# Kernel optimization log

Measured on AMD Instinct MI355X. Metric: run time of the kernel, lower is better.

## Reference

```python
import jax, jax.numpy as jnp
import numpy as np

E = 384      # EMBEDDING_SIZE
DFF = 1536
H = 6        # NUM_HEADS
D = E // H   # ATTN_DIM_SIZE = 64
T = 256      # SEQ_LEN
L = 6        # NUM_BLOCKS
V = 65       # VOCAB_SIZE
NPOS = 10000.0
B = 128


def _pos_encoding():
    i = jnp.arange(T, dtype=jnp.float32)[:, None]
    k = jnp.arange(E // 2, dtype=jnp.float32)[None, :]
    ang = i / jnp.power(NPOS, 2.0 * k / E)   # [T, E/2]
    pe = jnp.zeros((T, E), dtype=jnp.float32)
    pe = pe.at[:, 0::2].set(jnp.sin(ang))
    pe = pe.at[:, 1::2].set(jnp.cos(ang))
    return pe


def setup_inputs() -> dict:
    key = jax.random.key(0)
    ks = jax.random.split(key, 24)
    s = 0.02
    n = lambda k, shp: (jax.random.normal(k, shp, dtype=jnp.float32) * s)
    inp = {
        'tokens': jax.random.randint(ks[0], (B, T), 0, V),
        'pos_enc': _pos_encoding(),
        'emb': n(ks[1], (V, E)),
        # stacked per-layer params [L, ...]; weights stored as (in, out)
        'Wq': n(ks[2], (L, E, E)), 'bq': jnp.zeros((L, E)),
        'Wk': n(ks[3], (L, E, E)), 'bk': jnp.zeros((L, E)),
        'Wv': n(ks[4], (L, E, E)), 'bv': jnp.zeros((L, E)),
        'Wo': n(ks[5], (L, E, E)), 'bo': jnp.zeros((L, E)),
        'ln1_g': jnp.ones((L, E)), 'ln1_b': jnp.zeros((L, E)),
        'W1': n(ks[6], (L, E, DFF)), 'c1': jnp.zeros((L, DFF)),
        'W2': n(ks[7], (L, DFF, E)), 'c2': jnp.zeros((L, E)),
        'ln2_g': jnp.ones((L, E)), 'ln2_b': jnp.zeros((L, E)),
        'Wl': n(ks[8], (E, V)), 'bl': jnp.zeros((V,)),
    }
    return inp


def _layer_norm(x, g, b, eps=1e-5):
    mu = jnp.mean(x, axis=-1, keepdims=True)
    var = jnp.mean((x - mu) ** 2, axis=-1, keepdims=True)
    return (x - mu) * jax.lax.rsqrt(var + eps) * g + b


def _decoder(tokens, pos_enc, emb, Wq, bq, Wk, bk, Wv, bv, Wo, bo,
             ln1_g, ln1_b, W1, c1, W2, c2, ln2_g, ln2_b, Wl, bl):
    b_, t_ = tokens.shape
    x = emb[tokens] + pos_enc[None, :t_, :]            # [B,T,E]
    causal = jnp.tril(jnp.ones((t_, t_), dtype=bool)) # tril mask
    scale = D ** (-0.5)

    def block(x, p):
        (wq, bq_, wk, bk_, wv, bv_, wo, bo_, g1, be1, w1, c1_, w2, c2_, g2, be2) = p
        h = _layer_norm(x, g1, be1)
        q = (h @ wq + bq_).reshape(b_, t_, H, D)
        k = (h @ wk + bk_).reshape(b_, t_, H, D)
        v = (h @ wv + bv_).reshape(b_, t_, H, D)
        scores = jnp.einsum('bqhd,bkhd->bhqk', q, k) * scale
        scores = jnp.where(causal[None, None], scores, -jnp.inf)
        attn = jax.nn.softmax(scores, axis=-1)
        o = jnp.einsum('bhqk,bkhd->bqhd', attn, v).reshape(b_, t_, E)
        x = x + (o @ wo + bo_)
        h2 = _layer_norm(x, g2, be2)
        x = x + (jax.nn.relu(h2 @ w1 + c1_) @ w2 + c2_)
        return x, None

    params = (Wq, bq, Wk, bk, Wv, bv, Wo, bo, ln1_g, ln1_b, W1, c1, W2, c2, ln2_g, ln2_b)
    x, _ = jax.lax.scan(block, x, params)
    return x @ Wl + bl                                 # [B,T,V]


def reference(tokens, pos_enc, emb, Wq, bq, Wk, bk, Wv, bv, Wo, bo,
              ln1_g, ln1_b, W1, c1, W2, c2, ln2_g, ln2_b, Wl, bl):
    return _decoder(tokens, pos_enc, emb, Wq, bq, Wk, bk, Wv, bv, Wo, bo,
                    ln1_g, ln1_b, W1, c1, W2, c2, ln2_g, ln2_b, Wl, bl)
```

## Files before the change

kernel.cpp:

```cpp
#include <hip/hip_runtime.h>
#include <hip/hip_bf16.h>
#include <stdint.h>

constexpr int E   = 384;
constexpr int DFF = 1536;
constexpr int NH  = 6;
constexpr int HD  = 64;
constexpr int T   = 256;
constexpr int NL  = 6;
constexpr int NV  = 65;
constexpr int BB  = 128;
constexpr int MTOT = BB * T;
constexpr int CB  = 32;

typedef __bf16 bf16;
typedef __attribute__((ext_vector_type(8))) __bf16 bf16x8;
typedef __attribute__((ext_vector_type(4))) __bf16 bf16x4;
typedef __attribute__((ext_vector_type(4))) float floatx4;

__device__ __forceinline__ void gload_lds16(const void* g, void* l) {
    __builtin_amdgcn_global_load_lds(
        (const __attribute__((address_space(1))) void*)g,
        (__attribute__((address_space(3))) void*)l, 16, 0, 0);
}

#define GBM 128
#define GBN 128
#define GBK 64

template <int MODE, int SWAP>
__device__ __forceinline__ void gemm_body(
    char* AsB,
    const bf16* __restrict__ A, int lda,
    const bf16* __restrict__ Bf,
    const float* __restrict__ bias,
    void* __restrict__ Cv, void* __restrict__ Cv2, int ldc,
    int nt, int mt, int Nvalid, int K, int relu)
{
    int tid = threadIdx.x;
    int lane = tid & 63;
    int wid = tid >> 6;
    int wm = wid >> 2, wn = wid & 3;
    int lq = lane >> 4, lr = lane & 15;

    const bf16* Ab = A + (long)mt * GBM * lda;

    int srow = tid >> 3;
    int slot = tid & 7;
    int skc  = (slot ^ (srow & 7)) * 8;
    const bf16* Arow = Ab + (long)srow * lda + skc;
    const long a2 = 64 * (long)lda;
    int wofs = wid * 1024;

    int nk = K / GBK;
    int nks = K / 32;
    const bf16* Bq = Bf + ((long)(nt * 8 + wn * 2) * nks) * 512 + lane * 8;

    floatx4 zero = {0.f, 0.f, 0.f, 0.f};
    floatx4 acc[4][2];
#pragma unroll
    for (int i = 0; i < 4; i++)
#pragma unroll
        for (int j = 0; j < 2; j++) acc[i][j] = zero;

    const char* rp0 = AsB + (wm * 64 + lr) * 128;
    int rx0 = (lq * 16) ^ ((lr & 7) << 4);

    {
        char* base = AsB + wofs;
        gload_lds16(Arow,      base);
        gload_lds16(Arow + a2, base + 8192);
    }
    asm volatile("s_waitcnt vmcnt(0)" ::: "memory");
    __syncthreads();

    for (int ki = 0; ki < nk; ki++) {
        int ib = ki & 1;
        bf16x8 bb[4];
#pragma unroll
        for (int ni = 0; ni < 2; ni++)
#pragma unroll
            for (int kh = 0; kh < 2; kh++)
                bb[ni * 2 + kh] =
                    *(const bf16x8*)(Bq + ((long)ni * nks + 2 * ki + kh) * 512);
        if (ki + 1 < nk) {
            long koff = (long)(ki + 1) * GBK;
            char* base = AsB + (1 - ib) * 16384 + wofs;
            gload_lds16(Arow + koff,      base);
            gload_lds16(Arow + a2 + koff, base + 8192);
        }
        const char* rp = rp0 + ib * 16384;

        bf16x8 af[4];
#pragma unroll
        for (int mi = 0; mi < 4; mi++)
            af[mi] = *(const bf16x8*)(rp + mi * 2048 + rx0);
#pragma unroll
        for (int mi = 0; mi < 4; mi++)
#pragma unroll
            for (int ni = 0; ni < 2; ni++)
                acc[mi][ni] = SWAP
                    ? __builtin_amdgcn_mfma_f32_16x16x32_bf16(bb[ni * 2], af[mi], acc[mi][ni], 0, 0, 0)
                    : __builtin_amdgcn_mfma_f32_16x16x32_bf16(af[mi], bb[ni * 2], acc[mi][ni], 0, 0, 0);
#pragma unroll
        for (int mi = 0; mi < 4; mi++)
            af[mi] = *(const bf16x8*)(rp + mi * 2048 + (rx0 ^ 64));
#pragma unroll
        for (int mi = 0; mi < 4; mi++)
#pragma unroll
            for (int ni = 0; ni < 2; ni++)
                acc[mi][ni] = SWAP
                    ? __builtin_amdgcn_mfma_f32_16x16x32_bf16(bb[ni * 2 + 1], af[mi], acc[mi][ni], 0, 0, 0)
                    : __builtin_amdgcn_mfma_f32_16x16x32_bf16(af[mi], bb[ni * 2 + 1], acc[mi][ni], 0, 0, 0);
        __syncthreads();
    }

    int m0 = mt * GBM, n0 = nt * GBN;
#pragma unroll
    for (int mi = 0; mi < 4; mi++) {
#pragma unroll
        for (int ni = 0; ni < 2; ni++) {
            floatx4 v = acc[mi][ni];
            if (SWAP) {
                int rowL = m0 + wm * 64 + mi * 16 + lr;
                int col0 = n0 + wn * 32 + ni * 16 + lq * 4;
                if (MODE == 5) {
                    bf16x4 pv;
#pragma unroll
                    for (int r = 0; r < 4; r++) pv[r] = (bf16)(v[r] + bias[col0 + r]);
                    *(bf16x4*)((bf16*)Cv + (long)rowL * 768 + col0) = pv;
                } else if (MODE == 1) {
                    bf16* Cp = (bf16*)Cv;
                    bf16x4* ptr = (bf16x4*)(Cp + (long)rowL * ldc + col0);
                    bf16x4 old = *ptr;
                    bf16x4 pv;
#pragma unroll
                    for (int r = 0; r < 4; r++)
                        pv[r] = (bf16)((float)old[r] + v[r] + bias[col0 + r]);
                    *ptr = pv;
                } else if (MODE == 4) {
                    float* Cp = (float*)Cv;
#pragma unroll
                    for (int r = 0; r < 4; r++)
                        if (col0 + r < Nvalid)
                            Cp[(long)rowL * ldc + col0 + r] = v[r] + bias[col0 + r];
                } else {
                    if (col0 < Nvalid) {
                        bf16x4 pv;
#pragma unroll
                        for (int r = 0; r < 4; r++) {
                            float x = v[r] + (bias ? bias[col0 + r] : 0.f);
                            if (relu) x = fmaxf(x, 0.f);
                            pv[r] = (bf16)x;
                        }
                        *(bf16x4*)((bf16*)Cv + (long)rowL * ldc + col0) = pv;
                    }
                }
            } else {
                int row0 = m0 + wm * 64 + mi * 16 + lq * 4;
                int colL = n0 + wn * 32 + ni * 16 + lr;
                float bv = bias[colL];
                bf16x4 pv;
#pragma unroll
                for (int r = 0; r < 4; r++) pv[r] = (bf16)(v[r] + bv);
                int bidx = row0 >> 8, pos = row0 & 255, e = colL - 768;
                *(bf16x4*)((bf16*)Cv2 + (long)bidx * (E * T) + (long)e * T + pos) = pv;
            }
        }
    }
}

template <int MODE>
__global__ __launch_bounds__(512, 6) void k_gemm(
    const bf16* __restrict__ A, int lda,
    const bf16* __restrict__ Bf,
    const float* __restrict__ bias,
    void* __restrict__ Cv, void* __restrict__ Cv2, int ldc,
    int Mtiles, int Ntiles, int Nvalid, int K,
    int relu)
{
    __shared__ __align__(16) char AsB[2 * 16384];

    int nb = gridDim.x;
    int per = nb >> 3;
    int bphys = blockIdx.x;
    int bid = (bphys & 7) * per + (bphys >> 3);

    int nt = bid % Ntiles;
    int mt = bid / Ntiles;

    if (MODE == 5 && nt >= 6)
        gemm_body<5, 0>(AsB, A, lda, Bf, bias, Cv, Cv2, ldc, nt, mt, Nvalid, K, relu);
    else
        gemm_body<MODE, 1>(AsB, A, lda, Bf, bias, Cv, Cv2, ldc, nt, mt, Nvalid, K, relu);
}

__global__ __launch_bounds__(256) void k_attn(
    const bf16* __restrict__ qk, const bf16* __restrict__ vt,
    bf16* __restrict__ o)
{
    int nb = gridDim.x;
    int per = nb >> 3;
    int bphys = blockIdx.x;
    int bid = (bphys & 7) * per + (bphys >> 3);

    int qt = bid & 3; bid >>= 2;
    int h = bid % NH; int b = bid / NH;
    int tid = threadIdx.x;
    int lane = tid & 63;
    int w = tid >> 6;
    int lq = lane >> 4;
    int lr = lane & 15;

    __shared__ __align__(16) bf16 Ks[256 * 72];
    __shared__ __align__(16) bf16 Vs[64 * 264];

    const bf16* qbase = qk + (long)(b * T + qt * 64 + w * 16) * 768 + h * 64;
    const bf16* kbase = qk + (long)(b * T) * 768 + 384 + h * 64;
    const bf16* vbase = vt + ((long)b * E + h * 64) * T;

#pragma unroll
    for (int i = 0; i < 8; i++) {
        int idx = i * 256 + tid;
        int row = idx >> 3, off = (idx & 7) * 8;
        *(bf16x8*)(&Ks[row * 72 + off]) = *(const bf16x8*)(kbase + (long)row * 768 + off);
    }
#pragma unroll
    for (int i = 0; i < 8; i++) {
        int idx = i * 256 + tid;
        int row = idx >> 5, off = (idx & 31) * 8;
        *(bf16x8*)(&Vs[row * 264 + off]) = *(const bf16x8*)(vbase + (long)row * 256 + off);
    }

    bf16x8 aq0 = *(const bf16x8*)(qbase + (long)lr * 768 + lq * 8);
    bf16x8 aq1 = *(const bf16x8*)(qbase + (long)lr * 768 + 32 + lq * 8);

    __syncthreads();

    const int ntmax = qt * 4 + 3;
    floatx4 zero = {0.f, 0.f, 0.f, 0.f};
    floatx4 s[16];
#pragma unroll
    for (int nt = 0; nt < 16; nt++) s[nt] = zero;

#pragma unroll
    for (int nt = 0; nt < 16; nt++) {
        if (nt <= ntmax) {
            const bf16* kp = &Ks[(nt * 16 + lr) * 72 + lq * 8];
            bf16x8 b0 = *(const bf16x8*)(kp);
            bf16x8 b1 = *(const bf16x8*)(kp + 32);
            s[nt] = __builtin_amdgcn_mfma_f32_16x16x32_bf16(aq0, b0, s[nt], 0, 0, 0);
            s[nt] = __builtin_amdgcn_mfma_f32_16x16x32_bf16(aq1, b1, s[nt], 0, 0, 0);
        }
    }

    int trow0 = qt * 64 + w * 16 + lq * 4;
    float m4[4] = {-3e38f, -3e38f, -3e38f, -3e38f};
#pragma unroll
    for (int nt = 0; nt < 16; nt++) {
        if (nt <= ntmax) {
            int tc = nt * 16 + lr;
#pragma unroll
            for (int r = 0; r < 4; r++) {
                float v = s[nt][r] * 0.125f;
                if (tc > trow0 + r) v = -3e38f;
                s[nt][r] = v;
                m4[r] = fmaxf(m4[r], v);
            }
        }
    }
#pragma unroll
    for (int r = 0; r < 4; r++) {
#pragma unroll
        for (int off = 1; off < 16; off <<= 1)
            m4[r] = fmaxf(m4[r], __shfl_xor(m4[r], off, 64));
    }

    float l4[4] = {0.f, 0.f, 0.f, 0.f};
#pragma unroll
    for (int nt = 0; nt < 16; nt++) {
        if (nt <= ntmax) {
#pragma unroll
            for (int r = 0; r < 4; r++) {
                float pv = __expf(s[nt][r] - m4[r]);
                l4[r] += pv;
                s[nt][r] = pv;
            }
        }
    }
#pragma unroll
    for (int r = 0; r < 4; r++) {
#pragma unroll
        for (int off = 1; off < 16; off <<= 1)
            l4[r] += __shfl_xor(l4[r], off, 64);
    }

    __syncthreads();

    bf16* P = Ks + w * (16 * 264);
#pragma unroll
    for (int nt = 0; nt < 16; nt++) {
        if (nt <= ntmax) {
#pragma unroll
            for (int r = 0; r < 4; r++)
                P[(lq * 4 + r) * 264 + nt * 16 + lr] = (bf16)s[nt][r];
        }
    }

    floatx4 oacc[4];
#pragma unroll
    for (int nd = 0; nd < 4; nd++) oacc[nd] = zero;
    const int kkmax = 2 * (qt + 1);
#pragma unroll
    for (int kk = 0; kk < 8; kk++) {
        if (kk < kkmax) {
            bf16x8 ap = *(const bf16x8*)(&P[lr * 264 + kk * 32 + lq * 8]);
#pragma unroll
            for (int nd = 0; nd < 4; nd++) {
                bf16x8 bv = *(const bf16x8*)(&Vs[(nd * 16 + lr) * 264 + kk * 32 + lq * 8]);
                oacc[nd] = __builtin_amdgcn_mfma_f32_16x16x32_bf16(ap, bv, oacc[nd], 0, 0, 0);
            }
        }
    }

#pragma unroll
    for (int r = 0; r < 4; r++) {
        float inv = 1.0f / l4[r];
        long rowg = (long)b * T + trow0 + r;
#pragma unroll
        for (int nd = 0; nd < 4; nd++) {
            o[rowg * E + h * 64 + nd * 16 + lr] = (bf16)(oacc[nd][r] * inv);
        }
    }
}

__global__ void k_ln(const bf16* __restrict__ x, const float* __restrict__ g,
                     const float* __restrict__ b, bf16* __restrict__ h) {
    int row = blockIdx.x * 4 + (threadIdx.x >> 6);
    int lane = threadIdx.x & 63;
    const bf16* xr = x + (long)row * E;
    float v[6];
    float s = 0.f;
#pragma unroll
    for (int i = 0; i < 6; i++) { v[i] = (float)xr[lane + 64 * i]; s += v[i]; }
#pragma unroll
    for (int o = 1; o < 64; o <<= 1) s += __shfl_xor(s, o, 64);
    float mu = s * (1.0f / E);
    float q = 0.f;
#pragma unroll
    for (int i = 0; i < 6; i++) { float d = v[i] - mu; q += d * d; }
#pragma unroll
    for (int o = 1; o < 64; o <<= 1) q += __shfl_xor(q, o, 64);
    float rs = rsqrtf(q * (1.0f / E) + 1e-5f);
    bf16* hr = h + (long)row * E;
#pragma unroll
    for (int i = 0; i < 6; i++) {
        int c = lane + 64 * i;
        hr[c] = (bf16)((v[i] - mu) * rs * g[c] + b[c]);
    }
}

__global__ void k_transpose_frag(const float* __restrict__ W, bf16* __restrict__ Wf,
                                 int K, int N, int NPAD) {
    long idx = (long)blockIdx.x * 256 + threadIdx.x;
    long per = (long)NPAD * K;
    int l = (int)(idx / per);
    long r = idx - (long)l * per;
    int j = (int)(r & 7); r >>= 3;
    int lane = (int)(r & 63); r >>= 6;
    int nks = K / 32;
    int ks = (int)(r % nks);
    int c16 = (int)(r / nks);
    int col = c16 * 16 + (lane & 15);
    int k = ks * 32 + (lane >> 4) * 8 + j;
    Wf[idx] = (col < N) ? (bf16)W[((long)l * K + k) * N + col] : (bf16)0.0f;
}

__global__ void k_transpose_qkv_frag(const float* __restrict__ Wq, const float* __restrict__ Wk,
                                     const float* __restrict__ Wv, bf16* __restrict__ Wf) {
    long idx = (long)blockIdx.x * 256 + threadIdx.x;
    long per = (long)1152 * E;
    int l = (int)(idx / per);
    long r = idx - (long)l * per;
    int j = (int)(r & 7); r >>= 3;
    int lane = (int)(r & 63); r >>= 6;
    int nks = E / 32;
    int ks = (int)(r % nks);
    int c16 = (int)(r / nks);
    int col = c16 * 16 + (lane & 15);
    int k = ks * 32 + (lane >> 4) * 8 + j;
    const float* src;
    int cc;
    if (col < 384)      { src = Wq; cc = col; }
    else if (col < 768) { src = Wk; cc = col - 384; }
    else                { src = Wv; cc = col - 768; }
    Wf[idx] = (bf16)src[((long)l * E + k) * E + cc];
}

__global__ void k_bias_qkv(const float* __restrict__ bq, const float* __restrict__ bk,
                           const float* __restrict__ bv, float* __restrict__ bqkv) {
    int idx = blockIdx.x * 256 + threadIdx.x;
    int l = idx / 1152;
    int j = idx - l * 1152;
    const float* src;
    int jj;
    if (j < 384)      { src = bq; jj = j; }
    else if (j < 768) { src = bk; jj = j - 384; }
    else              { src = bv; jj = j - 768; }
    bqkv[idx] = src[l * E + jj];
}

__global__ void k_embed(const int* __restrict__ tokens, const float* __restrict__ pos,
                        const float* __restrict__ emb, bf16* __restrict__ x) {
    long idx = (long)blockIdx.x * 256 + threadIdx.x;
    int e = (int)(idx % E);
    long bt = idx / E;
    int t = (int)(bt % T);
    int tok = tokens[bt];
    x[idx] = (bf16)(emb[(long)tok * E + e] + pos[(long)t * E + e]);
}

extern "C" void kernel_launch(void* const* d_in, const int* in_sizes, int n_in,
                              void* d_out, int out_size, void* d_ws, size_t ws_size,
                              hipStream_t stream) {
    const int*   tokens = (const int*)d_in[0];
    const float* pos  = (const float*)d_in[1];
    const float* emb  = (const float*)d_in[2];
    const float* Wq   = (const float*)d_in[3];
    const float* bq   = (const float*)d_in[4];
    const float* Wk   = (const float*)d_in[5];
    const float* bk   = (const float*)d_in[6];
    const float* Wv   = (const float*)d_in[7];
    const float* bv   = (const float*)d_in[8];
    const float* Wo   = (const float*)d_in[9];
    const float* bo   = (const float*)d_in[10];
    const float* g1   = (const float*)d_in[11];
    const float* be1  = (const float*)d_in[12];
    const float* W1   = (const float*)d_in[13];
    const float* c1   = (const float*)d_in[14];
    const float* W2   = (const float*)d_in[15];
    const float* c2   = (const float*)d_in[16];
    const float* g2   = (const float*)d_in[17];
    const float* be2  = (const float*)d_in[18];
    const float* Wl   = (const float*)d_in[19];
    const float* bl   = (const float*)d_in[20];

    char* p = (char*)d_ws;
    bf16* x  = (bf16*)p;   p += (long)MTOT * E * 2;
    bf16* h  = (bf16*)p;   p += (long)MTOT * E * 2;
    bf16* qk = (bf16*)p;   p += (long)MTOT * 768 * 2;
    bf16* vt = (bf16*)p;   p += (long)BB * E * T * 2;
    bf16* SP = (bf16*)p;   p += (long)CB * NH * T * T * 2;
    bf16* WqkvF = (bf16*)p; p += (long)NL * 1152 * E * 2;
    bf16* WoF = (bf16*)p;  p += (long)NL * E * E * 2;
    bf16* W1F = (bf16*)p;  p += (long)NL * DFF * E * 2;
    bf16* W2F = (bf16*)p;  p += (long)NL * E * DFF * 2;
    bf16* WlF = (bf16*)p;  p += (long)128 * E * 2;
    float* bqkv = (float*)p; p += (long)NL * 1152 * 4;
    bf16* mid = qk;
    bf16* o   = h;
    (void)SP;

    k_transpose_qkv_frag<<<(NL * 1152 * E) / 256, 256, 0, stream>>>(Wq, Wk, Wv, WqkvF);
    k_transpose_frag<<<(NL * E * E) / 256, 256, 0, stream>>>(Wo, WoF, E, E, E);
    k_transpose_frag<<<(NL * DFF * E) / 256, 256, 0, stream>>>(W1, W1F, E, DFF, DFF);
    k_transpose_frag<<<(NL * E * DFF) / 256, 256, 0, stream>>>(W2, W2F, DFF, E, E);
    k_transpose_frag<<<(128 * E) / 256, 256, 0, stream>>>(Wl, WlF, E, NV, 128);
    k_bias_qkv<<<(NL * 1152) / 256, 256, 0, stream>>>(bq, bk, bv, bqkv);

    k_embed<<<(MTOT * E) / 256, 256, 0, stream>>>(tokens, pos, emb, x);

    for (int l = 0; l < NL; l++) {
        k_ln<<<MTOT / 4, 256, 0, stream>>>(x, g1 + l * E, be1 + l * E, h);
        k_gemm<5><<<256 * 9, 512, 0, stream>>>(h, E, WqkvF + (long)l * 1152 * E,
                                               bqkv + l * 1152, qk, vt, 0,
                                               256, 9, 1152, E, 0);
        k_attn<<<BB * NH * 4, 256, 0, stream>>>(qk, vt, o);
        k_gemm<1><<<256 * 3, 512, 0, stream>>>(o, E, WoF + (long)l * E * E,
                                               bo + l * E, x, nullptr, E,
                                               256, 3, E, E, 0);
        k_ln<<<MTOT / 4, 256, 0, stream>>>(x, g2 + l * E, be2 + l * E, h);
        k_gemm<0><<<256 * 12, 512, 0, stream>>>(h, E, W1F + (long)l * DFF * E,
                                                c1 + l * DFF, mid, nullptr, DFF,
                                                256, 12, DFF, E, 1);
        k_gemm<1><<<256 * 3, 512, 0, stream>>>(mid, DFF, W2F + (long)l * E * DFF,
                                               c2 + l * E, x, nullptr, E,
                                               256, 3, E, DFF, 0);
    }

    k_gemm<4><<<256 * 1, 512, 0, stream>>>(x, E, WlF,
                                           bl, d_out, nullptr, NV,
                                           256, 1, NV, E, 0);
}
```

Before: 1.676 ms.

## Enlarge GEMM M-tile to 256 with 4x2 wave grid and 64x64 warp tiles

Doubles the GEMM block tile from 128x128 to 256x128 and remaps the eight waves to a 4x2 grid, so each wave computes a 64x64 sub-tile with 16 accumulators instead of 8. The B fragments are now loaded in two halves per k-step to limit register use, and the LDS double buffer doubles to 64KB. The aim is more reuse of each B load and fewer blocks, lowering global traffic per FLOP. In exchange, register and LDS pressure rise (occupancy hint lowered to 4) and the grid halves, which may leave fewer waves to hide latency.

```diff
diff --git a/kernel.cpp b/kernel.cpp
--- a/kernel.cpp
+++ b/kernel.cpp
@@ -24,7 +24,7 @@
         (__attribute__((address_space(3))) void*)l, 16, 0, 0);
 }
 
-#define GBM 128
+#define GBM 256
 #define GBN 128
 #define GBK 64
 
@@ -40,7 +40,7 @@
     int tid = threadIdx.x;
     int lane = tid & 63;
     int wid = tid >> 6;
-    int wm = wid >> 2, wn = wid & 3;
+    int wr = wid >> 1, wc = wid & 1;
     int lq = lane >> 4, lr = lane & 15;
 
     const bf16* Ab = A + (long)mt * GBM * lda;
@@ -54,23 +54,20 @@
 
     int nk = K / GBK;
     int nks = K / 32;
-    const bf16* Bq = Bf + ((long)(nt * 8 + wn * 2) * nks) * 512 + lane * 8;
-
-    floatx4 zero = {0.f, 0.f, 0.f, 0.f};
-    floatx4 acc[4][2];
+    const bf16* Bq = Bf + ((long)(nt * 8 + wc * 4) * nks) * 512 + lane * 8;
+
+    floatx4 acc[4][4];
 #pragma unroll
     for (int i = 0; i < 4; i++)
 #pragma unroll
-        for (int j = 0; j < 2; j++) acc[i][j] = zero;
-
-    const char* rp0 = AsB + (wm * 64 + lr) * 128;
+        for (int j = 0; j < 4; j++) acc[i][j] = floatx4{0.f, 0.f, 0.f, 0.f};
+
+    const char* rp0 = AsB + (wr * 64 + lr) * 128;
     int rx0 = (lq * 16) ^ ((lr & 7) << 4);
 
-    {
-        char* base = AsB + wofs;
-        gload_lds16(Arow,      base);
-        gload_lds16(Arow + a2, base + 8192);
-    }
+#pragma unroll
+    for (int g = 0; g < 4; g++)
+        gload_lds16(Arow + g * a2, AsB + wofs + g * 8192);
     asm volatile("s_waitcnt vmcnt(0)" ::: "memory");
     __syncthreads();
 
@@ -78,18 +75,16 @@
         int ib = ki & 1;
         bf16x8 bb[4];
 #pragma unroll
-        for (int ni = 0; ni < 2; ni++)
-#pragma unroll
-            for (int kh = 0; kh < 2; kh++)
-                bb[ni * 2 + kh] =
-                    *(const bf16x8*)(Bq + ((long)ni * nks + 2 * ki + kh) * 512);
+        for (int ni = 0; ni < 4; ni++)
+            bb[ni] = *(const bf16x8*)(Bq + ((long)ni * nks + 2 * ki) * 512);
         if (ki + 1 < nk) {
             long koff = (long)(ki + 1) * GBK;
-            char* base = AsB + (1 - ib) * 16384 + wofs;
-            gload_lds16(Arow + koff,      base);
-            gload_lds16(Arow + a2 + koff, base + 8192);
-        }
-        const char* rp = rp0 + ib * 16384;
+            char* base = AsB + (1 - ib) * 32768 + wofs;
+#pragma unroll
+            for (int g = 0; g < 4; g++)
+                gload_lds16(Arow + g * a2 + koff, base + g * 8192);
+        }
+        const char* rp = rp0 + ib * 32768;
 
         bf16x8 af[4];
 #pragma unroll
@@ -98,20 +93,23 @@
 #pragma unroll
         for (int mi = 0; mi < 4; mi++)
 #pragma unroll
-            for (int ni = 0; ni < 2; ni++)
+            for (int ni = 0; ni < 4; ni++)
                 acc[mi][ni] = SWAP
-                    ? __builtin_amdgcn_mfma_f32_16x16x32_bf16(bb[ni * 2], af[mi], acc[mi][ni], 0, 0, 0)
-                    : __builtin_amdgcn_mfma_f32_16x16x32_bf16(af[mi], bb[ni * 2], acc[mi][ni], 0, 0, 0);
+                    ? __builtin_amdgcn_mfma_f32_16x16x32_bf16(bb[ni], af[mi], acc[mi][ni], 0, 0, 0)
+                    : __builtin_amdgcn_mfma_f32_16x16x32_bf16(af[mi], bb[ni], acc[mi][ni], 0, 0, 0);
+#pragma unroll
+        for (int ni = 0; ni < 4; ni++)
+            bb[ni] = *(const bf16x8*)(Bq + ((long)ni * nks + 2 * ki + 1) * 512);
 #pragma unroll
         for (int mi = 0; mi < 4; mi++)
             af[mi] = *(const bf16x8*)(rp + mi * 2048 + (rx0 ^ 64));
 #pragma unroll
         for (int mi = 0; mi < 4; mi++)
 #pragma unroll
-            for (int ni = 0; ni < 2; ni++)
+            for (int ni = 0; ni < 4; ni++)
                 acc[mi][ni] = SWAP
-                    ? __builtin_amdgcn_mfma_f32_16x16x32_bf16(bb[ni * 2 + 1], af[mi], acc[mi][ni], 0, 0, 0)
-                    : __builtin_amdgcn_mfma_f32_16x16x32_bf16(af[mi], bb[ni * 2 + 1], acc[mi][ni], 0, 0, 0);
+                    ? __builtin_amdgcn_mfma_f32_16x16x32_bf16(bb[ni], af[mi], acc[mi][ni], 0, 0, 0)
+                    : __builtin_amdgcn_mfma_f32_16x16x32_bf16(af[mi], bb[ni], acc[mi][ni], 0, 0, 0);
         __syncthreads();
     }
 
@@ -119,11 +117,11 @@
 #pragma unroll
     for (int mi = 0; mi < 4; mi++) {
 #pragma unroll
-        for (int ni = 0; ni < 2; ni++) {
+        for (int ni = 0; ni < 4; ni++) {
             floatx4 v = acc[mi][ni];
             if (SWAP) {
-                int rowL = m0 + wm * 64 + mi * 16 + lr;
-                int col0 = n0 + wn * 32 + ni * 16 + lq * 4;
+                int rowL = m0 + wr * 64 + mi * 16 + lr;
+                int col0 = n0 + wc * 64 + ni * 16 + lq * 4;
                 if (MODE == 5) {
                     bf16x4 pv;
 #pragma unroll
@@ -157,8 +155,8 @@
                     }
                 }
             } else {
-                int row0 = m0 + wm * 64 + mi * 16 + lq * 4;
-                int colL = n0 + wn * 32 + ni * 16 + lr;
+                int row0 = m0 + wr * 64 + mi * 16 + lq * 4;
+                int colL = n0 + wc * 64 + ni * 16 + lr;
                 float bv = bias[colL];
                 bf16x4 pv;
 #pragma unroll
@@ -171,7 +169,7 @@
 }
 
 template <int MODE>
-__global__ __launch_bounds__(512, 6) void k_gemm(
+__global__ __launch_bounds__(512, 4) void k_gemm(
     const bf16* __restrict__ A, int lda,
     const bf16* __restrict__ Bf,
     const float* __restrict__ bias,
@@ -179,7 +177,7 @@
     int Mtiles, int Ntiles, int Nvalid, int K,
     int relu)
 {
-    __shared__ __align__(16) char AsB[2 * 16384];
+    __shared__ __align__(16) char AsB[2 * 32768];
 
     int nb = gridDim.x;
     int per = nb >> 3;
@@ -472,23 +470,23 @@
 
     for (int l = 0; l < NL; l++) {
         k_ln<<<MTOT / 4, 256, 0, stream>>>(x, g1 + l * E, be1 + l * E, h);
-        k_gemm<5><<<256 * 9, 512, 0, stream>>>(h, E, WqkvF + (long)l * 1152 * E,
+        k_gemm<5><<<128 * 9, 512, 0, stream>>>(h, E, WqkvF + (long)l * 1152 * E,
                                                bqkv + l * 1152, qk, vt, 0,
-                                               256, 9, 1152, E, 0);
+                                               128, 9, 1152, E, 0);
         k_attn<<<BB * NH * 4, 256, 0, stream>>>(qk, vt, o);
-        k_gemm<1><<<256 * 3, 512, 0, stream>>>(o, E, WoF + (long)l * E * E,
+        k_gemm<1><<<128 * 3, 512, 0, stream>>>(o, E, WoF + (long)l * E * E,
                                                bo + l * E, x, nullptr, E,
-                                               256, 3, E, E, 0);
+                                               128, 3, E, E, 0);
         k_ln<<<MTOT / 4, 256, 0, stream>>>(x, g2 + l * E, be2 + l * E, h);
-        k_gemm<0><<<256 * 12, 512, 0, stream>>>(h, E, W1F + (long)l * DFF * E,
+        k_gemm<0><<<128 * 12, 512, 0, stream>>>(h, E, W1F + (long)l * DFF * E,
                                                 c1 + l * DFF, mid, nullptr, DFF,
-                                                256, 12, DFF, E, 1);
-        k_gemm<1><<<256 * 3, 512, 0, stream>>>(mid, DFF, W2F + (long)l * E * DFF,
+                                                128, 12, DFF, E, 1);
+        k_gemm<1><<<128 * 3, 512, 0, stream>>>(mid, DFF, W2F + (long)l * E * DFF,
                                                c2 + l * E, x, nullptr, E,
-                                               256, 3, E, DFF, 0);
-    }
-
-    k_gemm<4><<<256 * 1, 512, 0, stream>>>(x, E, WlF,
+                                               128, 3, E, DFF, 0);
+    }
+
+    k_gemm<4><<<128 * 1, 512, 0, stream>>>(x, E, WlF,
                                            bl, d_out, nullptr, NV,
-                                           256, 1, NV, E, 0);
-}
+                                           128, 1, NV, E, 0);
+}
```

Result: slower. 1.893 ms (+12.9%).
